# Kernel tuning notes

Measured on AMD Instinct MI355X. Metric: run time of the kernel, lower is better.

Reference implementation:

```python
import jax, jax.numpy as jnp
import numpy as np

B, T, D = 4, 2048, 1024
H = 16            # N_HEADS
HD = D // H       # head_dim = 64
VD = 64           # VALUE_DIM


def setup_inputs() -> dict:
    key = jax.random.key(0)
    ks = jax.random.split(key, 9)
    s_in = 1.0 / np.sqrt(D)
    s_out = 1.0 / np.sqrt(H * VD)
    x = jax.random.normal(ks[0], (B, T, D), dtype=jnp.float32)
    # stacked per-head projection weights (nn.Linear applies x @ W.T; we store [in,out])
    Wq = jax.random.uniform(ks[1], (H, D, HD), jnp.float32, -s_in, s_in)
    bq = jax.random.uniform(ks[2], (H, HD), jnp.float32, -s_in, s_in)
    Wk = jax.random.uniform(ks[3], (H, D, HD), jnp.float32, -s_in, s_in)
    bk = jax.random.uniform(ks[4], (H, HD), jnp.float32, -s_in, s_in)
    Wv = jax.random.uniform(ks[5], (H, D, VD), jnp.float32, -s_in, s_in)
    bv = jax.random.uniform(ks[6], (H, VD), jnp.float32, -s_in, s_in)
    Wo = jax.random.uniform(ks[7], (H * VD, D), jnp.float32, -s_out, s_out)
    bo = jax.random.uniform(ks[8], (D,), jnp.float32, -s_out, s_out)
    return {"x": x, "Wq": Wq, "bq": bq, "Wk": Wk, "bk": bk,
            "Wv": Wv, "bv": bv, "Wo": Wo, "bo": bo}


def reference(x, Wq, bq, Wk, bk, Wv, bv, Wo, bo):
    b, t, d = x.shape
    scale = HD ** -0.5
    # per-head projections, vectorized over heads
    q = jnp.einsum('btd,hdk->bhtk', x, Wq) + bq[None, :, None, :]
    k = jnp.einsum('btd,hdk->bhtk', x, Wk) + bk[None, :, None, :]
    v = jnp.einsum('btd,hdv->bhtv', x, Wv) + bv[None, :, None, :]
    scores = jnp.einsum('bhsk,bhtk->bhst', q, k) * scale
    causal = jnp.triu(jnp.ones((t, t), dtype=bool), k=1)  # mask[i,j]=j>i
    scores = jnp.where(causal, -jnp.inf, scores)
    attn = jax.nn.softmax(scores, axis=-1)  # dropout = identity in eval
    out = jnp.einsum('bhst,bhtv->bhsv', attn, v)
    concat = out.transpose(0, 2, 1, 3).reshape(b, t, H * VD)  # cat over heads
    return concat @ Wo + bo
```

## Files before the change

### kernel.cpp

```cpp
#include <hip/hip_runtime.h>

#define Bc 4
#define Tc 2048
#define Dc 1024
#define Hc 16
#define HDc 64
#define VDc 64
#define MTOT (Bc * Tc)
#define NQKV 3072

typedef __attribute__((ext_vector_type(8))) short short8;
typedef __attribute__((ext_vector_type(4))) short short4_;
typedef __attribute__((ext_vector_type(4))) float float4_;

#define QSCALE 0.18033688011112042f

static __device__ __forceinline__ short f2bf(float f) {
  unsigned u = __builtin_bit_cast(unsigned, f);
  u += 0x7fffu + ((u >> 16) & 1u);
  return (short)(u >> 16);
}

static __device__ __forceinline__ void gload16(const void* g, void* l) {
  __builtin_amdgcn_global_load_lds(
      (__attribute__((address_space(1))) void*)(unsigned long long)g,
      (__attribute__((address_space(3))) void*)l, 16, 0, 0);
}


__global__ void cvt_x_kernel(const float* __restrict__ x, short* __restrict__ xb) {
  int i = blockIdx.x * blockDim.x + threadIdx.x;
  float4_ v = reinterpret_cast<const float4_*>(x)[i];
  short4_ o;
  o[0] = f2bf(v[0]); o[1] = f2bf(v[1]); o[2] = f2bf(v[2]); o[3] = f2bf(v[3]);
  reinterpret_cast<short4_*>(xb)[i] = o;
}

__global__ __launch_bounds__(256) void build_wqkv_kernel(
    const float* __restrict__ Wq, const float* __restrict__ Wk,
    const float* __restrict__ Wv, const float* __restrict__ bq,
    const float* __restrict__ bk, const float* __restrict__ bv,
    short* __restrict__ wt, float* __restrict__ bias) {
  __shared__ __align__(16) short Lt[64][72];
  const int tid = threadIdx.x;
  const int mat = blockIdx.x >> 4, h = blockIdx.x & 15;
  const float* W  = (mat == 0) ? Wq : (mat == 1) ? Wk : Wv;
  const float* bs = (mat == 0) ? bq : (mat == 1) ? bk : bv;
  const int base_n = (mat << 10) + (h << 6);
  if (blockIdx.y == 0 && tid < 64) bias[base_n + tid] = bs[h * 64 + tid];
  for (int dc = 0; dc < 4; dc++) {
    const int d0 = blockIdx.y * 256 + dc * 64;
#pragma unroll
    for (int rep = 0; rep < 16; rep++) {
      int dl = rep * 4 + (tid >> 6);
      int hd = tid & 63;
      Lt[hd][dl] = f2bf(W[(size_t)(h * 1024 + d0 + dl) * 64 + hd]);
    }
    __syncthreads();
    int hd = tid >> 2, c = tid & 3;
    short8 v0 = *(const short8*)&Lt[hd][c * 16];
    short8 v1 = *(const short8*)&Lt[hd][c * 16 + 8];
    *(short8*)&wt[(size_t)(base_n + hd) * 1024 + d0 + c * 16] = v0;
    *(short8*)&wt[(size_t)(base_n + hd) * 1024 + d0 + c * 16 + 8] = v1;
    __syncthreads();
  }
}

__global__ __launch_bounds__(256) void build_wo_kernel(
    const float* __restrict__ Wo, short* __restrict__ wot) {
  __shared__ __align__(16) short Lt[64][72];
  const int tid = threadIdx.x;
  const int n0 = blockIdx.x * 64, k0 = blockIdx.y * 64;
#pragma unroll
  for (int rep = 0; rep < 16; rep++) {
    int kl = rep * 4 + (tid >> 6);
    int nl = tid & 63;
    Lt[nl][kl] = f2bf(Wo[(size_t)(k0 + kl) * 1024 + n0 + nl]);
  }
  __syncthreads();
  int nl = tid >> 2, c = tid & 3;
  short8 v0 = *(const short8*)&Lt[nl][c * 16];
  short8 v1 = *(const short8*)&Lt[nl][c * 16 + 8];
  *(short8*)&wot[(size_t)(n0 + nl) * 1024 + k0 + c * 16] = v0;
  *(short8*)&wot[(size_t)(n0 + nl) * 1024 + k0 + c * 16 + 8] = v1;
}

#define GEMM_KLOOP(SHSZ)                                                       \
  __shared__ __align__(16) short Sh[SHSZ];                                     \
  const int tid = threadIdx.x;                                                 \
  const int wave = tid >> 6, lane = tid & 63;                                  \
  const int lm = lane & 15, quad = lane >> 4;                                  \
  const int wm = (wave & 1) * 64, wn = (wave >> 1) * 64;                       \
  const int srow = tid >> 2, pchunk = tid & 3;                                 \
  const int swr = (srow ^ (srow >> 2)) & 3;                                    \
  const int pq = quad ^ ((lm ^ (lm >> 2)) & 3);                                \
  const short* Ag = A + (size_t)(m0 + srow) * 1024 + (pchunk ^ swr) * 8;       \
  const short* Bg = Bt + (size_t)(n0 + srow) * 1024 + (pchunk ^ swr) * 8;      \
  float4_ acc[4][4] = {};                                                      \
  gload16(Ag, &Sh[wave * 512]);                                                \
  gload16(Ag + 64 * 1024, &Sh[2048 + wave * 512]);                             \
  gload16(Bg, &Sh[4096 + wave * 512]);                                         \
  gload16(Bg + 64 * 1024, &Sh[6144 + wave * 512]);                             \
  for (int k0 = 0; k0 < 1024; k0 += 32) {                                      \
    const int cb = (k0 >> 5) & 1;                                              \
    __syncthreads();                                                           \
    if (k0 + 32 < 1024) {                                                      \
      short* d = &Sh[(1 - cb) * 8192];                                         \
      gload16(Ag + k0 + 32, d + wave * 512);                                   \
      gload16(Ag + 64 * 1024 + k0 + 32, d + 2048 + wave * 512);                \
      gload16(Bg + k0 + 32, d + 4096 + wave * 512);                            \
      gload16(Bg + 64 * 1024 + k0 + 32, d + 6144 + wave * 512);                \
    }                                                                          \
    const short* Ab = &Sh[cb * 8192];                                          \
    const short* Bb = &Sh[cb * 8192 + 4096];                                   \
    short8 af[4], bf[4];                                                       \
    _Pragma("unroll") for (int i = 0; i < 4; i++) {                            \
      af[i] = *(const short8*)&Ab[(wm + i * 16 + lm) * 32 + pq * 8];           \
      bf[i] = *(const short8*)&Bb[(wn + i * 16 + lm) * 32 + pq * 8];           \
    }                                                                          \
    _Pragma("unroll") for (int i = 0; i < 4; i++)                              \
      _Pragma("unroll") for (int j = 0; j < 4; j++)                            \
        acc[i][j] = __builtin_amdgcn_mfma_f32_16x16x32_bf16(af[i], bf[j],      \
                                                            acc[i][j], 0, 0, 0); \
  }

__global__ __launch_bounds__(256) void gemm_qkv_kernel(
    const short* __restrict__ A, const short* __restrict__ Bt,
    const float* __restrict__ bias,
    short* __restrict__ Qb, short* __restrict__ Kb, short* __restrict__ Vt) {
  const int m0 = blockIdx.x * 128, n0 = blockIdx.y * 128;
  GEMM_KLOOP(18432)
  __syncthreads();
  short* epi = &Sh[wave * 4608];
  const int mat = n0 >> 10;
  const int hh = ((n0 + wn) >> 6) & 15;
  const int b = m0 >> 11;
  const int bh = b * Hc + hh;
  const int t0 = (m0 & (Tc - 1)) + wm;
  if (mat < 2) {
    const float sc = (mat == 0) ? QSCALE : 1.0f;
#pragma unroll
    for (int j = 0; j < 4; j++) {
      float bvs = bias[n0 + wn + j * 16 + lm] * sc;
#pragma unroll
      for (int i = 0; i < 4; i++)
#pragma unroll
        for (int r = 0; r < 4; r++)
          epi[(i * 16 + quad * 4 + r) * 72 + j * 16 + lm] = f2bf(acc[i][j][r] * sc + bvs);
    }
    __asm__ volatile("s_waitcnt lgkmcnt(0)" ::: "memory");
    short* dst = (mat == 0) ? Qb : Kb;
#pragma unroll
    for (int p = 0; p < 8; p++) {
      int lrow = p * 8 + (lane >> 3);
      short8 v = *(const short8*)&epi[lrow * 72 + (lane & 7) * 8];
      *(short8*)&dst[((size_t)bh * Tc + t0 + lrow) * HDc + (lane & 7) * 8] = v;
    }
  } else {
#pragma unroll
    for (int j = 0; j < 4; j++) {
      float bv = bias[n0 + wn + j * 16 + lm];
#pragma unroll
      for (int i = 0; i < 4; i++) {
        short4_ pk;
#pragma unroll
        for (int r = 0; r < 4; r++) pk[r] = f2bf(acc[i][j][r] + bv);
        *(short4_*)&epi[(j * 16 + lm) * 72 + i * 16 + quad * 4] = pk;
      }
    }
    __asm__ volatile("s_waitcnt lgkmcnt(0)" ::: "memory");
#pragma unroll
    for (int p = 0; p < 8; p++) {
      int hdrow = p * 8 + (lane >> 3);
      short8 v = *(const short8*)&epi[hdrow * 72 + (lane & 7) * 8];
      *(short8*)&Vt[((size_t)bh * VDc + hdrow) * Tc + t0 + (lane & 7) * 8] = v;
    }
  }
}

__global__ __launch_bounds__(256) void gemm_out_kernel(
    const short* __restrict__ A, const short* __restrict__ Bt,
    const float* __restrict__ bo, float* __restrict__ out) {
  const int m0 = blockIdx.x * 128, n0 = blockIdx.y * 128;
  GEMM_KLOOP(16384)
#pragma unroll
  for (int j = 0; j < 4; j++) {
    int n = n0 + wn + j * 16 + lm;
    float bv = bo[n];
#pragma unroll
    for (int i = 0; i < 4; i++) {
#pragma unroll
      for (int r = 0; r < 4; r++) {
        int m = m0 + wm + i * 16 + quad * 4 + r;
        out[(size_t)m * Dc + n] = acc[i][j][r] + bv;
      }
    }
  }
}

__global__ __launch_bounds__(512) void attn_kernel(
    const short* __restrict__ Qb, const short* __restrict__ Kb,
    const short* __restrict__ Vt, short* __restrict__ AO) {
  __shared__ __align__(16) short Ks[2][64 * 64];
  __shared__ __align__(16) short Vs[2][64 * 64];
  __shared__ __align__(16) short Pbuf[8][32 * 64];
  const int tid = threadIdx.x;
  const int wave = tid >> 6, lane = tid & 63;
  const int lm = lane & 15, quad = lane >> 4;
  const int bh = blockIdx.y;
  const int qblk = (blockIdx.y < 32) ? (7 - blockIdx.x) : blockIdx.x;
  const int q0 = qblk * 256 + wave * 32;

  const short* Qp = Qb + (size_t)bh * Tc * HDc;
  const short* Kp = Kb + (size_t)bh * Tc * HDc;
  const short* Vp = Vt + (size_t)bh * VDc * Tc;
  short* pb = Pbuf[wave];

  const int srow = tid >> 3;
  const int chlog = (tid & 7) ^ (srow & 7);
  const int sw = lm & 7;

  short8 qf[2][2];
#pragma unroll
  for (int g = 0; g < 2; g++)
#pragma unroll
    for (int h = 0; h < 2; h++)
      qf[g][h] = *reinterpret_cast<const short8*>(Qp + (q0 + g * 16 + lm) * HDc + h * 32 + quad * 8);

  float4_ o[4][2] = {};
  float lsum[2] = {0.f, 0.f};

  const int nt = 4 * qblk + 4;
  gload16(Kp + (size_t)srow * HDc + chlog * 8, &Ks[0][wave * 512]);
  gload16(Vp + (size_t)srow * Tc + chlog * 8, &Vs[0][wave * 512]);

  for (int it = 0; it < nt; ++it) {
    const int kt = it << 6;
    const int cur = it & 1;
    __syncthreads();
    if (it + 1 < nt) {
      const int ktn = kt + 64;
      gload16(Kp + (size_t)(ktn + srow) * HDc + chlog * 8, &Ks[1 - cur][wave * 512]);
      gload16(Vp + (size_t)srow * Tc + ktn + chlog * 8, &Vs[1 - cur][wave * 512]);
    }
    if (kt > q0 + 31) continue;
    const short* Kt = Ks[cur];
    const short* Vtl = Vs[cur];

    float4_ st[4][2] = {};
#pragma unroll
    for (int mf = 0; mf < 4; ++mf) {
      int row = mf * 16 + lm;
      short8 k0 = *(const short8*)&Kt[row * 64 + (quad ^ sw) * 8];
      short8 k1 = *(const short8*)&Kt[row * 64 + ((4 + quad) ^ sw) * 8];
#pragma unroll
      for (int g = 0; g < 2; ++g) {
        st[mf][g] = __builtin_amdgcn_mfma_f32_16x16x32_bf16(k0, qf[g][0], st[mf][g], 0, 0, 0);
        st[mf][g] = __builtin_amdgcn_mfma_f32_16x16x32_bf16(k1, qf[g][1], st[mf][g], 0, 0, 0);
      }
    }

    if (kt + 63 > q0) {
#pragma unroll
      for (int mf = 0; mf < 4; ++mf)
#pragma unroll
        for (int g = 0; g < 2; ++g) {
          int qrow = q0 + g * 16 + lm;
#pragma unroll
          for (int r = 0; r < 4; ++r) {
            int key = kt + mf * 16 + quad * 4 + r;
            if (key > qrow) st[mf][g][r] = -1e30f;
          }
        }
    }

#pragma unroll
    for (int g = 0; g < 2; ++g) {
      float sum = 0.f;
#pragma unroll
      for (int mf = 0; mf < 4; ++mf) {
        float p0 = __builtin_amdgcn_exp2f(st[mf][g][0]);
        float p1 = __builtin_amdgcn_exp2f(st[mf][g][1]);
        float p2 = __builtin_amdgcn_exp2f(st[mf][g][2]);
        float p3 = __builtin_amdgcn_exp2f(st[mf][g][3]);
        sum += (p0 + p1) + (p2 + p3);
        short4_ pk;
        pk[0] = f2bf(p0); pk[1] = f2bf(p1); pk[2] = f2bf(p2); pk[3] = f2bf(p3);
        *(short4_*)&pb[(g * 16 + lm) * 64 + ((mf * 2 + (quad >> 1)) ^ sw) * 8 + (quad & 1) * 4] = pk;
      }
      lsum[g] += sum;
    }
    __asm__ volatile("s_waitcnt lgkmcnt(0)" ::: "memory");

    short8 pf[2][2];
#pragma unroll
    for (int g = 0; g < 2; ++g)
#pragma unroll
      for (int h = 0; h < 2; ++h)
        pf[g][h] = *reinterpret_cast<const short8*>(&pb[(g * 16 + lm) * 64 + ((h * 4 + quad) ^ sw) * 8]);

#pragma unroll
    for (int mf2 = 0; mf2 < 4; ++mf2) {
      int row = mf2 * 16 + lm;
      short8 v0 = *(const short8*)&Vtl[row * 64 + (quad ^ sw) * 8];
      short8 v1 = *(const short8*)&Vtl[row * 64 + ((4 + quad) ^ sw) * 8];
#pragma unroll
      for (int g = 0; g < 2; ++g) {
        o[mf2][g] = __builtin_amdgcn_mfma_f32_16x16x32_bf16(v0, pf[g][0], o[mf2][g], 0, 0, 0);
        o[mf2][g] = __builtin_amdgcn_mfma_f32_16x16x32_bf16(v1, pf[g][1], o[mf2][g], 0, 0, 0);
      }
    }
  }

#pragma unroll
  for (int g = 0; g < 2; ++g) {
    lsum[g] += __shfl_xor(lsum[g], 16);
    lsum[g] += __shfl_xor(lsum[g], 32);
  }

  const int b = bh >> 4, h = bh & 15;
  float inv0 = 1.0f / lsum[0], inv1 = 1.0f / lsum[1];
#pragma unroll
  for (int g = 0; g < 2; ++g) {
    float inv = g ? inv1 : inv0;
#pragma unroll
    for (int mf2 = 0; mf2 < 4; ++mf2) {
      short4_ pk;
      pk[0] = f2bf(o[mf2][g][0] * inv); pk[1] = f2bf(o[mf2][g][1] * inv);
      pk[2] = f2bf(o[mf2][g][2] * inv); pk[3] = f2bf(o[mf2][g][3] * inv);
      *(short4_*)&pb[(g * 16 + lm) * 64 + ((mf2 * 2 + (quad >> 1)) ^ sw) * 8 + (quad & 1) * 4] = pk;
    }
  }
  __asm__ volatile("s_waitcnt lgkmcnt(0)" ::: "memory");
#pragma unroll
  for (int p = 0; p < 4; ++p) {
    int lr = p * 8 + (lane >> 3);
    short8 vv = *reinterpret_cast<const short8*>(&pb[lr * 64 + (((lane & 7) ^ (lr & 7))) * 8]);
    *reinterpret_cast<short8*>(AO + ((size_t)(b * Tc + q0 + lr)) * 1024 + h * 64 + (lane & 7) * 8) = vv;
  }
}

extern "C" void kernel_launch(void* const* d_in, const int* in_sizes, int n_in,
                              void* d_out, int out_size, void* d_ws, size_t ws_size,
                              hipStream_t stream) {
  const float* x  = (const float*)d_in[0];
  const float* Wq = (const float*)d_in[1];
  const float* bq = (const float*)d_in[2];
  const float* Wk = (const float*)d_in[3];
  const float* bk = (const float*)d_in[4];
  const float* Wv = (const float*)d_in[5];
  const float* bv = (const float*)d_in[6];
  const float* Wo = (const float*)d_in[7];
  const float* bo = (const float*)d_in[8];
  float* out = (float*)d_out;

  char* ws = (char*)d_ws;
  size_t off = 0;
  short* xb   = (short*)(ws + off); off += (size_t)MTOT * Dc * 2;
  short* wqkv = (short*)(ws + off); off += (size_t)NQKV * Dc * 2;
  float* bqkv = (float*)(ws + off); off += ((size_t)NQKV * 4 + 255) & ~255ull;
  short* Qb   = (short*)(ws + off); off += (size_t)Bc * Hc * Tc * HDc * 2;
  short* Kb   = (short*)(ws + off); off += (size_t)Bc * Hc * Tc * HDc * 2;
  short* Vt   = (short*)(ws + off); off += (size_t)Bc * Hc * VDc * Tc * 2;
  short* AO   = (short*)(ws + off); off += (size_t)MTOT * 1024 * 2;
  short* wot  = (short*)(ws + off); off += (size_t)Dc * Dc * 2;

  cvt_x_kernel<<<MTOT * Dc / (256 * 4), 256, 0, stream>>>(x, xb);
  build_wqkv_kernel<<<dim3(48, 4), 256, 0, stream>>>(Wq, Wk, Wv, bq, bk, bv, wqkv, bqkv);
  build_wo_kernel<<<dim3(16, 16), 256, 0, stream>>>(Wo, wot);
  gemm_qkv_kernel<<<dim3(MTOT / 128, NQKV / 128), 256, 0, stream>>>(xb, wqkv, bqkv, Qb, Kb, Vt);
  attn_kernel<<<dim3(8, Bc * Hc), 512, 0, stream>>>(Qb, Kb, Vt, AO);
  gemm_out_kernel<<<dim3(MTOT / 128, Dc / 128), 256, 0, stream>>>(AO, wot, bo, out);
}
```

Baseline: 256.9 us.

## Keep softmax probabilities in registers and widen attention waves to 64 queries

The attention kernel now runs 4 waves of 256 threads per block instead of 8, with each wave owning 64 query rows rather than 32. Each K/V tile loaded into shared memory is therefore reused across more queries per wave. The P matrix no longer takes a round trip through the per-wave LDS buffer. Probabilities are packed to bf16 with a cheap perm-based rounding and fed straight into the PV MFMA as the B operand, with V fragments read in a matching permuted order. The trade-off is a larger register footprint (more accumulators and packed P) and fewer, more serial waves per block, which could cut occupancy or cause spills.

```diff
diff --git a/kernel.cpp b/kernel.cpp
--- a/kernel.cpp
+++ b/kernel.cpp
@@ -12,6 +12,7 @@
 typedef __attribute__((ext_vector_type(8))) short short8;
 typedef __attribute__((ext_vector_type(4))) short short4_;
 typedef __attribute__((ext_vector_type(4))) float float4_;
+typedef __attribute__((ext_vector_type(4))) unsigned uint4_;
 
 #define QSCALE 0.18033688011112042f
 
@@ -19,6 +20,11 @@
   unsigned u = __builtin_bit_cast(unsigned, f);
   u += 0x7fffu + ((u >> 16) & 1u);
   return (short)(u >> 16);
+}
+static __device__ __forceinline__ unsigned packp(float a, float b) {
+  unsigned ua = __builtin_bit_cast(unsigned, a) + 0x8000u;
+  unsigned ub = __builtin_bit_cast(unsigned, b) + 0x8000u;
+  return __builtin_amdgcn_perm(ub, ua, 0x07060302);
 }
 
 static __device__ __forceinline__ void gload16(const void* g, void* l) {
@@ -198,41 +204,42 @@
   }
 }
 
-__global__ __launch_bounds__(512) void attn_kernel(
+__global__ __launch_bounds__(256, 2) void attn_kernel(
     const short* __restrict__ Qb, const short* __restrict__ Kb,
     const short* __restrict__ Vt, short* __restrict__ AO) {
-  __shared__ __align__(16) short Ks[2][64 * 64];
-  __shared__ __align__(16) short Vs[2][64 * 64];
-  __shared__ __align__(16) short Pbuf[8][32 * 64];
+  __shared__ __align__(16) short Sh[16384];
   const int tid = threadIdx.x;
   const int wave = tid >> 6, lane = tid & 63;
   const int lm = lane & 15, quad = lane >> 4;
   const int bh = blockIdx.y;
   const int qblk = (blockIdx.y < 32) ? (7 - blockIdx.x) : blockIdx.x;
-  const int q0 = qblk * 256 + wave * 32;
+  const int q0 = qblk * 256 + wave * 64;
 
   const short* Qp = Qb + (size_t)bh * Tc * HDc;
   const short* Kp = Kb + (size_t)bh * Tc * HDc;
   const short* Vp = Vt + (size_t)bh * VDc * Tc;
-  short* pb = Pbuf[wave];
 
   const int srow = tid >> 3;
   const int chlog = (tid & 7) ^ (srow & 7);
   const int sw = lm & 7;
 
-  short8 qf[2][2];
-#pragma unroll
-  for (int g = 0; g < 2; g++)
+  short8 qf[4][2];
+#pragma unroll
+  for (int g = 0; g < 4; g++)
 #pragma unroll
     for (int h = 0; h < 2; h++)
-      qf[g][h] = *reinterpret_cast<const short8*>(Qp + (q0 + g * 16 + lm) * HDc + h * 32 + quad * 8);
-
-  float4_ o[4][2] = {};
-  float lsum[2] = {0.f, 0.f};
+      qf[g][h] = *(const short8*)&Qp[(q0 + g * 16 + lm) * HDc + h * 32 + quad * 8];
+
+  float4_ o[4][4] = {};
+  float lsum[4] = {};
+  unsigned pk[4][4][2];
 
   const int nt = 4 * qblk + 4;
-  gload16(Kp + (size_t)srow * HDc + chlog * 8, &Ks[0][wave * 512]);
-  gload16(Vp + (size_t)srow * Tc + chlog * 8, &Vs[0][wave * 512]);
+#pragma unroll
+  for (int c = 0; c < 2; c++) {
+    gload16(Kp + (size_t)(c * 32 + srow) * HDc + chlog * 8, &Sh[c * 2048 + wave * 512]);
+    gload16(Vp + (size_t)(c * 32 + srow) * Tc + chlog * 8, &Sh[8192 + c * 2048 + wave * 512]);
+  }
 
   for (int it = 0; it < nt; ++it) {
     const int kt = it << 6;
@@ -240,103 +247,101 @@
     __syncthreads();
     if (it + 1 < nt) {
       const int ktn = kt + 64;
-      gload16(Kp + (size_t)(ktn + srow) * HDc + chlog * 8, &Ks[1 - cur][wave * 512]);
-      gload16(Vp + (size_t)srow * Tc + ktn + chlog * 8, &Vs[1 - cur][wave * 512]);
-    }
-    if (kt > q0 + 31) continue;
-    const short* Kt = Ks[cur];
-    const short* Vtl = Vs[cur];
-
-    float4_ st[4][2] = {};
+      const int nb = (1 - cur) * 4096;
+#pragma unroll
+      for (int c = 0; c < 2; c++) {
+        gload16(Kp + (size_t)(ktn + c * 32 + srow) * HDc + chlog * 8, &Sh[nb + c * 2048 + wave * 512]);
+        gload16(Vp + (size_t)(c * 32 + srow) * Tc + ktn + chlog * 8, &Sh[8192 + nb + c * 2048 + wave * 512]);
+      }
+    }
+    if (kt > q0 + 63) continue;
+    const short* Kt = &Sh[cur * 4096];
+    const short* Vtl = &Sh[8192 + cur * 4096];
+    const bool diag = (kt + 63 > q0);
+
 #pragma unroll
     for (int mf = 0; mf < 4; ++mf) {
       int row = mf * 16 + lm;
       short8 k0 = *(const short8*)&Kt[row * 64 + (quad ^ sw) * 8];
       short8 k1 = *(const short8*)&Kt[row * 64 + ((4 + quad) ^ sw) * 8];
-#pragma unroll
-      for (int g = 0; g < 2; ++g) {
-        st[mf][g] = __builtin_amdgcn_mfma_f32_16x16x32_bf16(k0, qf[g][0], st[mf][g], 0, 0, 0);
-        st[mf][g] = __builtin_amdgcn_mfma_f32_16x16x32_bf16(k1, qf[g][1], st[mf][g], 0, 0, 0);
-      }
-    }
-
-    if (kt + 63 > q0) {
-#pragma unroll
-      for (int mf = 0; mf < 4; ++mf)
-#pragma unroll
-        for (int g = 0; g < 2; ++g) {
+      float4_ st[4];
+#pragma unroll
+      for (int g = 0; g < 4; ++g) {
+        float4_ s = {};
+        s = __builtin_amdgcn_mfma_f32_16x16x32_bf16(k0, qf[g][0], s, 0, 0, 0);
+        s = __builtin_amdgcn_mfma_f32_16x16x32_bf16(k1, qf[g][1], s, 0, 0, 0);
+        st[g] = s;
+      }
+      if (diag) {
+#pragma unroll
+        for (int g = 0; g < 4; ++g) {
           int qrow = q0 + g * 16 + lm;
 #pragma unroll
-          for (int r = 0; r < 4; ++r) {
-            int key = kt + mf * 16 + quad * 4 + r;
-            if (key > qrow) st[mf][g][r] = -1e30f;
-          }
+          for (int r = 0; r < 4; ++r)
+            if (kt + mf * 16 + quad * 4 + r > qrow) st[g][r] = -1e30f;
         }
-    }
-
-#pragma unroll
-    for (int g = 0; g < 2; ++g) {
-      float sum = 0.f;
-#pragma unroll
-      for (int mf = 0; mf < 4; ++mf) {
-        float p0 = __builtin_amdgcn_exp2f(st[mf][g][0]);
-        float p1 = __builtin_amdgcn_exp2f(st[mf][g][1]);
-        float p2 = __builtin_amdgcn_exp2f(st[mf][g][2]);
-        float p3 = __builtin_amdgcn_exp2f(st[mf][g][3]);
-        sum += (p0 + p1) + (p2 + p3);
-        short4_ pk;
-        pk[0] = f2bf(p0); pk[1] = f2bf(p1); pk[2] = f2bf(p2); pk[3] = f2bf(p3);
-        *(short4_*)&pb[(g * 16 + lm) * 64 + ((mf * 2 + (quad >> 1)) ^ sw) * 8 + (quad & 1) * 4] = pk;
-      }
-      lsum[g] += sum;
-    }
-    __asm__ volatile("s_waitcnt lgkmcnt(0)" ::: "memory");
-
-    short8 pf[2][2];
-#pragma unroll
-    for (int g = 0; g < 2; ++g)
-#pragma unroll
-      for (int h = 0; h < 2; ++h)
-        pf[g][h] = *reinterpret_cast<const short8*>(&pb[(g * 16 + lm) * 64 + ((h * 4 + quad) ^ sw) * 8]);
-
+      }
+#pragma unroll
+      for (int g = 0; g < 4; ++g) {
+        float p0 = __builtin_amdgcn_exp2f(st[g][0]);
+        float p1 = __builtin_amdgcn_exp2f(st[g][1]);
+        float p2 = __builtin_amdgcn_exp2f(st[g][2]);
+        float p3 = __builtin_amdgcn_exp2f(st[g][3]);
+        lsum[g] += (p0 + p1) + (p2 + p3);
+        pk[mf][g][0] = packp(p0, p1);
+        pk[mf][g][1] = packp(p2, p3);
+      }
+    }
+
+#pragma unroll
+    for (int h = 0; h < 2; ++h) {
+      short8 bfr[4];
+#pragma unroll
+      for (int g = 0; g < 4; ++g) {
+        uint4_ bu = {pk[2 * h][g][0], pk[2 * h][g][1], pk[2 * h + 1][g][0], pk[2 * h + 1][g][1]};
+        bfr[g] = __builtin_bit_cast(short8, bu);
+      }
+#pragma unroll
+      for (int mf2 = 0; mf2 < 4; ++mf2) {
+        int row = mf2 * 16 + lm;
+        short4_ va = *(const short4_*)&Vtl[row * 64 + ((4 * h + (quad >> 1)) ^ sw) * 8 + (quad & 1) * 4];
+        short4_ vb = *(const short4_*)&Vtl[row * 64 + ((4 * h + 2 + (quad >> 1)) ^ sw) * 8 + (quad & 1) * 4];
+        short8 af = __builtin_shufflevector(va, vb, 0, 1, 2, 3, 4, 5, 6, 7);
+#pragma unroll
+        for (int g = 0; g < 4; ++g)
+          o[mf2][g] = __builtin_amdgcn_mfma_f32_16x16x32_bf16(af, bfr[g], o[mf2][g], 0, 0, 0);
+      }
+    }
+  }
+
+  float inv[4];
+#pragma unroll
+  for (int g = 0; g < 4; ++g) {
+    float s = lsum[g];
+    s += __shfl_xor(s, 16);
+    s += __shfl_xor(s, 32);
+    inv[g] = 1.0f / s;
+  }
+
+  __syncthreads();
+  const int b = bh >> 4, h = bh & 15;
+  short* epi = &Sh[wave * 4096];
+#pragma unroll
+  for (int g = 0; g < 4; ++g) {
 #pragma unroll
     for (int mf2 = 0; mf2 < 4; ++mf2) {
-      int row = mf2 * 16 + lm;
-      short8 v0 = *(const short8*)&Vtl[row * 64 + (quad ^ sw) * 8];
-      short8 v1 = *(const short8*)&Vtl[row * 64 + ((4 + quad) ^ sw) * 8];
-#pragma unroll
-      for (int g = 0; g < 2; ++g) {
-        o[mf2][g] = __builtin_amdgcn_mfma_f32_16x16x32_bf16(v0, pf[g][0], o[mf2][g], 0, 0, 0);
-        o[mf2][g] = __builtin_amdgcn_mfma_f32_16x16x32_bf16(v1, pf[g][1], o[mf2][g], 0, 0, 0);
-      }
-    }
-  }
-
-#pragma unroll
-  for (int g = 0; g < 2; ++g) {
-    lsum[g] += __shfl_xor(lsum[g], 16);
-    lsum[g] += __shfl_xor(lsum[g], 32);
-  }
-
-  const int b = bh >> 4, h = bh & 15;
-  float inv0 = 1.0f / lsum[0], inv1 = 1.0f / lsum[1];
-#pragma unroll
-  for (int g = 0; g < 2; ++g) {
-    float inv = g ? inv1 : inv0;
-#pragma unroll
-    for (int mf2 = 0; mf2 < 4; ++mf2) {
-      short4_ pk;
-      pk[0] = f2bf(o[mf2][g][0] * inv); pk[1] = f2bf(o[mf2][g][1] * inv);
-      pk[2] = f2bf(o[mf2][g][2] * inv); pk[3] = f2bf(o[mf2][g][3] * inv);
-      *(short4_*)&pb[(g * 16 + lm) * 64 + ((mf2 * 2 + (quad >> 1)) ^ sw) * 8 + (quad & 1) * 4] = pk;
+      short4_ pkv;
+      pkv[0] = f2bf(o[mf2][g][0] * inv[g]); pkv[1] = f2bf(o[mf2][g][1] * inv[g]);
+      pkv[2] = f2bf(o[mf2][g][2] * inv[g]); pkv[3] = f2bf(o[mf2][g][3] * inv[g]);
+      *(short4_*)&epi[(g * 16 + lm) * 64 + ((2 * mf2 + (quad >> 1)) ^ sw) * 8 + (quad & 1) * 4] = pkv;
     }
   }
   __asm__ volatile("s_waitcnt lgkmcnt(0)" ::: "memory");
 #pragma unroll
-  for (int p = 0; p < 4; ++p) {
+  for (int p = 0; p < 8; ++p) {
     int lr = p * 8 + (lane >> 3);
-    short8 vv = *reinterpret_cast<const short8*>(&pb[lr * 64 + (((lane & 7) ^ (lr & 7))) * 8]);
-    *reinterpret_cast<short8*>(AO + ((size_t)(b * Tc + q0 + lr)) * 1024 + h * 64 + (lane & 7) * 8) = vv;
+    short8 vv = *(const short8*)&epi[lr * 64 + ((lane & 7) ^ (lr & 7)) * 8];
+    *(short8*)&AO[((size_t)(b * Tc + q0 + lr)) * 1024 + h * 64 + (lane & 7) * 8] = vv;
   }
 }
 
@@ -369,6 +374,6 @@
   build_wqkv_kernel<<<dim3(48, 4), 256, 0, stream>>>(Wq, Wk, Wv, bq, bk, bv, wqkv, bqkv);
   build_wo_kernel<<<dim3(16, 16), 256, 0, stream>>>(Wo, wot);
   gemm_qkv_kernel<<<dim3(MTOT / 128, NQKV / 128), 256, 0, stream>>>(xb, wqkv, bqkv, Qb, Kb, Vt);
-  attn_kernel<<<dim3(8, Bc * Hc), 512, 0, stream>>>(Qb, Kb, Vt, AO);
+  attn_kernel<<<dim3(8, Bc * Hc), 256, 0, stream>>>(Qb, Kb, Vt, AO);
   gemm_out_kernel<<<dim3(MTOT / 128, Dc / 128), 256, 0, stream>>>(AO, wot, bo, out);
 }
```

Measured after the change: 246.4 us. -4.1%, faster.
